# Optimization experiments

Measured on AMD Instinct MI355X. Metric: run time of the kernel, lower is better.

Reference implementation:

```python
import jax, jax.numpy as jnp
import numpy as np

NN_SIZE = 16  # nn_size from __init__


def _knn_idx(points_ref, k):
    """Brute-force KNN of points_ref against itself (replaces faiss_knn).
    Returns (B, N, k) neighbor indices, self point excluded."""
    sq = jnp.sum(points_ref * points_ref, axis=-1)  # (B, N)
    # squared pairwise distances (B, N, N)
    d2 = sq[:, :, None] + sq[:, None, :] - 2.0 * jnp.einsum(
        'bnd,bmd->bnm', points_ref, points_ref)
    _, idx = jax.lax.top_k(-d2, k + 1)  # nearest first; idx[...,0] is self
    return idx[:, :, 1:]


def _edge_lengths(pts, knn_idx):
    """Gather neighbor coords and compute edge lengths (B, N, K)."""
    group = jax.vmap(lambda p, i: p[i])(pts, knn_idx)  # (B, N, K, D)
    return jnp.linalg.norm(group - pts[:, :, None, :], axis=-1)


def setup_inputs() -> dict:
    key = jax.random.key(0)
    k1, k2 = jax.random.split(key)
    B, N, D = 4, 8192, 3
    points_ref = jax.random.normal(k1, (B, N, D), dtype=jnp.float32)
    # pred points: perturbed ref so the loss is non-degenerate
    points = points_ref + 0.01 * jax.random.normal(k2, (B, N, D), dtype=jnp.float32)
    return {"points_ref": points_ref, "points": points}


def reference(points_ref, points):
    # faiss KNN is non-differentiable -> stop_gradient on the index search
    knn_idx = _knn_idx(jax.lax.stop_gradient(points_ref), NN_SIZE)  # (B,N,K)
    dist_ref = _edge_lengths(points_ref, knn_idx)  # (B, N, K)
    dist = _edge_lengths(points, knn_idx)          # (B, N, K)
    # metric = torch.nn.L1Loss() (mean reduction)
    return jnp.mean(jnp.abs(dist_ref - dist))
```

## Files before the change

### kernel.cpp

```cpp
#include <hip/hip_runtime.h>
#include <math.h>

#define BATCH 4
#define NPTS  8192
#define KNN   16
#define KK    17
#define QPB   32
#define SPLITS 8
#define BLOCK 256
#define RANGE (NPTS/SPLITS)
#define SAMPLE 128
#define AL    8
#define CAP   32
#define CHUNK 8
#define TOTAL_EDGES (BATCH*NPTS*KNN)

__global__ void pel_pack(const float* __restrict__ pref, const float* __restrict__ pts,
                         float4* __restrict__ p4r, float4* __restrict__ p4p,
                         float* __restrict__ acc) {
    if (blockIdx.x == 0 && threadIdx.x == 0) acc[0] = 0.0f;
    const int idx = blockIdx.x * blockDim.x + threadIdx.x;
    const int n = BATCH * NPTS;
    if (idx < n) {
        float x = pref[3*idx], y = pref[3*idx+1], z = pref[3*idx+2];
        p4r[idx] = make_float4(x, y, z, fmaf(x, x, fmaf(y, y, z*z)));
        x = pts[3*idx]; y = pts[3*idx+1]; z = pts[3*idx+2];
        p4p[idx] = make_float4(x, y, z, fmaf(x, x, fmaf(y, y, z*z)));
    }
}

__global__ void pel_finalize(const float* __restrict__ acc, float* __restrict__ out) {
    out[0] = acc[0] * (1.0f / (float)TOTAL_EDGES);
}

__device__ __forceinline__ float cand_e4(const float4 p, float xi, float yi, float zi) {
    return fmaf(-2.0f, fmaf(p.x, xi, fmaf(p.y, yi, p.z * zi)), p.w);
}

__global__ __launch_bounds__(BLOCK, 4)
void pel_main(const float4* __restrict__ P4r, const float4* __restrict__ P4p,
              float* __restrict__ acc_ws)
{
    __shared__ float s_c17[KK][BLOCK];
    __shared__ unsigned short s_bufJ[CAP][BLOCK];
    __shared__ float s_tau[QPB];
    __shared__ float s_part[BLOCK / 64];

    const int t  = threadIdx.x;
    const int lq = t & (QPB - 1);
    const int sp = t >> 5;
    const int q  = blockIdx.x * QPB + lq;
    const int b  = q >> 13;
    const int i  = q & (NPTS - 1);

    const float4* __restrict__ Pq = P4r + b * NPTS;
    const float4* __restrict__ Pp = P4p + b * NPTS;

    const float4 self = Pq[i];
    const float xi = self.x, yi = self.y, zi = self.z, sqi = self.w;
    const int base = sp * RANGE;
    const float4* __restrict__ Pb = Pq + base;

    float al[AL];
    #pragma unroll
    for (int k = 0; k < AL; ++k) al[k] = 3.0e38f;
    for (int j0 = 0; j0 < SAMPLE; j0 += CHUNK) {
        float4 c[CHUNK];
        #pragma unroll
        for (int u = 0; u < CHUNK; ++u) c[u] = Pb[j0 + u];
        #pragma unroll
        for (int u = 0; u < CHUNK; ++u) {
            const float e = cand_e4(c[u], xi, yi, zi);
            if (e < al[AL-1]) {
                #pragma unroll
                for (int k = AL-1; k >= 1; --k) al[k] = fminf(al[k], fmaxf(al[k-1], e));
                al[0] = fminf(al[0], e);
            }
        }
    }
    #pragma unroll
    for (int k = 0; k < AL; ++k) s_c17[k][t] = al[k];
    __syncthreads();

    if (t < 64) {
        const int mq = t & 31, half = t >> 5;
        float m[KK];
        #pragma unroll
        for (int k = 0; k < KK; ++k) m[k] = 3.0e38f;
        for (int s = 0; s < SPLITS/2; ++s) {
            const int r = mq + (half * (SPLITS/2) + s) * QPB;
            for (int k = 0; k < AL; ++k) {
                const float c = s_c17[k][r];
                if (c >= m[KK-1]) break;
                #pragma unroll
                for (int kk = KK-1; kk >= 1; --kk) m[kk] = fminf(m[kk], fmaxf(m[kk-1], c));
                m[0] = fminf(m[0], c);
            }
        }
        float tau = -3.0e38f;
        #pragma unroll
        for (int k = 0; k < KK; ++k) {
            const float bk = __shfl(m[KK-1-k], mq + 32, 64);
            tau = fmaxf(tau, fminf(m[k], bk));
        }
        if (half == 0) s_tau[mq] = tau;
    }
    __syncthreads();
    float tauL = s_tau[lq];

    int cnt = 0;
    for (int j0 = 0; j0 < RANGE; j0 += CHUNK) {
        float4 c[CHUNK];
        #pragma unroll
        for (int u = 0; u < CHUNK; ++u) c[u] = Pb[j0 + u];
        #pragma unroll
        for (int u = 0; u < CHUNK; ++u) {
            const float e = cand_e4(c[u], xi, yi, zi);
            if (e <= tauL) {
                s_bufJ[cnt][t] = (unsigned short)(base + j0 + u);
                if (++cnt == CAP) {
                    float c17[KK];
                    #pragma unroll
                    for (int k = 0; k < KK; ++k) c17[k] = 3.0e38f;
                    for (int n = 0; n < CAP; ++n) {
                        const float ee = cand_e4(Pq[s_bufJ[n][t]], xi, yi, zi);
                        if (ee < c17[KK-1]) {
                            #pragma unroll
                            for (int k = KK-1; k >= 1; --k) c17[k] = fminf(c17[k], fmaxf(c17[k-1], ee));
                            c17[0] = fminf(c17[0], ee);
                        }
                    }
                    const float th = c17[KK-1];
                    int kept = 0;
                    for (int n = 0; n < CAP; ++n) {
                        const unsigned short jj = s_bufJ[n][t];
                        const float ee = cand_e4(Pq[jj], xi, yi, zi);
                        if (ee <= th) { s_bufJ[kept][t] = jj; ++kept; }
                    }
                    cnt = kept;
                    tauL = fminf(tauL, th);
                }
            }
        }
    }

    {
        float c17[KK];
        #pragma unroll
        for (int k = 0; k < KK; ++k) c17[k] = 3.0e38f;
        for (int n = 0; n < cnt; ++n) {
            const float ee = cand_e4(Pq[s_bufJ[n][t]], xi, yi, zi);
            if (ee < c17[KK-1]) {
                #pragma unroll
                for (int k = KK-1; k >= 1; --k) c17[k] = fminf(c17[k], fmaxf(c17[k-1], ee));
                c17[0] = fminf(c17[0], ee);
            }
        }
        #pragma unroll
        for (int k = 0; k < KK; ++k) s_c17[k][t] = c17[k];
    }
    __syncthreads();
    if (t < 64) {
        const int mq = t & 31, half = t >> 5;
        float m[KK];
        #pragma unroll
        for (int k = 0; k < KK; ++k) m[k] = 3.0e38f;
        for (int s = 0; s < SPLITS/2; ++s) {
            const int r = mq + (half * (SPLITS/2) + s) * QPB;
            for (int k = 0; k < KK; ++k) {
                const float c = s_c17[k][r];
                if (c >= m[KK-1]) break;
                #pragma unroll
                for (int kk = KK-1; kk >= 1; --kk) m[kk] = fminf(m[kk], fmaxf(m[kk-1], c));
                m[0] = fminf(m[0], c);
            }
        }
        float tau = -3.0e38f;
        #pragma unroll
        for (int k = 0; k < KK; ++k) {
            const float bk = __shfl(m[KK-1-k], mq + 32, 64);
            tau = fmaxf(tau, fminf(m[k], bk));
        }
        if (half == 0) s_tau[mq] = tau;
    }
    __syncthreads();
    const float tau = s_tau[lq];

    const float4 selfp = Pp[i];
    float acc = 0.0f;
    for (int n = 0; n < cnt; ++n) {
        const int jj = s_bufJ[n][t];
        const float ee = cand_e4(Pq[jj], xi, yi, zi);
        if (ee <= tau) {
            const float d2r = fmaxf(ee + sqi, 0.0f);
            const float ep  = cand_e4(Pp[jj], selfp.x, selfp.y, selfp.z);
            const float d2p = fmaxf(ep + selfp.w, 0.0f);
            acc += fabsf(sqrtf(d2r) - sqrtf(d2p));
        }
    }

    #pragma unroll
    for (int off = 32; off > 0; off >>= 1) acc += __shfl_down(acc, off, 64);
    if ((t & 63) == 0) s_part[t >> 6] = acc;
    __syncthreads();
    if (t == 0) {
        float s = 0.0f;
        #pragma unroll
        for (int w = 0; w < BLOCK / 64; ++w) s += s_part[w];
        atomicAdd(acc_ws, s);
    }
}

extern "C" void kernel_launch(void* const* d_in, const int* in_sizes, int n_in,
                              void* d_out, int out_size, void* d_ws, size_t ws_size,
                              hipStream_t stream) {
    const float* pref = (const float*)d_in[0];
    const float* pts  = (const float*)d_in[1];
    float*  wsf = (float*)d_ws;
    float*  acc = wsf;
    float4* P4r = (float4*)(wsf + 4);
    float4* P4p = P4r + BATCH * NPTS;
    float*  out = (float*)d_out;

    const int n = BATCH * NPTS;
    pel_pack<<<(n + 255) / 256, 256, 0, stream>>>(pref, pts, P4r, P4p, acc);
    pel_main<<<n / QPB, BLOCK, 0, stream>>>(P4r, P4p, acc);
    pel_finalize<<<1, 1, 0, stream>>>(acc, out);
}
```

Before: 302.8 us.

## Pack distance and index into sortable keys, branchless candidate buffering, fuse finalize

Candidates become 32-bit keys: the float squared distance with its low 13 mantissa bits replaced by the point index. This lets the top-k lists carry indices directly, so the rescans that reloaded points to recompute distances go away, and the final pass only visits the 17 kept keys. The filter pass writes every key to shared memory and advances the counter without a branch, compacting once the buffer nears capacity. The block shrinks to 16 queries (128 threads), and the finalize kernel is folded into the main kernel through a last-block counter. The truncated mantissa can change neighbor choice on near ties, and unconditional shared stores add write traffic.

```diff
diff --git a/kernel.cpp b/kernel.cpp
--- a/kernel.cpp
+++ b/kernel.cpp
@@ -5,23 +5,26 @@
 #define NPTS  8192
 #define KNN   16
 #define KK    17
-#define QPB   32
+#define QPB   16
 #define SPLITS 8
-#define BLOCK 256
+#define BLOCK (QPB*SPLITS)
 #define RANGE (NPTS/SPLITS)
 #define SAMPLE 128
 #define AL    8
-#define CAP   32
+#define CAP   30
 #define CHUNK 8
+#define NQ    (BATCH*NPTS)
+#define GRID  (NQ/QPB)
+#define JMASK 0x1FFFu
+#define EMASK 0xFFFFE000u
 #define TOTAL_EDGES (BATCH*NPTS*KNN)
 
 __global__ void pel_pack(const float* __restrict__ pref, const float* __restrict__ pts,
                          float4* __restrict__ p4r, float4* __restrict__ p4p,
-                         float* __restrict__ acc) {
-    if (blockIdx.x == 0 && threadIdx.x == 0) acc[0] = 0.0f;
+                         float* __restrict__ acc, unsigned* __restrict__ bcnt) {
+    if (blockIdx.x == 0 && threadIdx.x == 0) { acc[0] = 0.0f; bcnt[0] = 0u; }
     const int idx = blockIdx.x * blockDim.x + threadIdx.x;
-    const int n = BATCH * NPTS;
-    if (idx < n) {
+    if (idx < NQ) {
         float x = pref[3*idx], y = pref[3*idx+1], z = pref[3*idx+2];
         p4r[idx] = make_float4(x, y, z, fmaf(x, x, fmaf(y, y, z*z)));
         x = pts[3*idx]; y = pts[3*idx+1]; z = pts[3*idx+2];
@@ -29,26 +32,50 @@
     }
 }
 
-__global__ void pel_finalize(const float* __restrict__ acc, float* __restrict__ out) {
-    out[0] = acc[0] * (1.0f / (float)TOTAL_EDGES);
-}
-
-__device__ __forceinline__ float cand_e4(const float4 p, float xi, float yi, float zi) {
-    return fmaf(-2.0f, fmaf(p.x, xi, fmaf(p.y, yi, p.z * zi)), p.w);
+__device__ __forceinline__ unsigned mkkey(const float4 p, float xi, float yi,
+                                          float zi, float sqi, unsigned j) {
+    const float dot = fmaf(p.x, xi, fmaf(p.y, yi, p.z * zi));
+    const float d2  = fmaf(-2.0f, dot, p.w) + sqi;
+    return (__float_as_uint(d2) & EMASK) | j;
+}
+
+template<int RL>
+__device__ __forceinline__ unsigned merge_tau(const unsigned (*s_key)[BLOCK], int t) {
+    const int mq = t & (QPB - 1), half = t >> 4;
+    unsigned m[KK];
+    #pragma unroll
+    for (int k = 0; k < KK; ++k) m[k] = 0xFFFFFFFFu;
+    for (int s = (SPLITS/2) * half; s < (SPLITS/2) * (half + 1); ++s) {
+        const int col = mq + s * QPB;
+        for (int k = 0; k < RL; ++k) {
+            const unsigned c = s_key[k][col];
+            if (c >= m[KK-1]) break;
+            #pragma unroll
+            for (int kk = KK-1; kk >= 1; --kk) m[kk] = min(m[kk], max(m[kk-1], c));
+            m[0] = min(m[0], c);
+        }
+    }
+    unsigned tau = 0;
+    #pragma unroll
+    for (int k = 0; k < KK; ++k) {
+        const unsigned bk = (unsigned)__shfl((int)m[KK-1-k], t ^ 16, 64);
+        tau = max(tau, min(m[k], bk));
+    }
+    return tau;
 }
 
 __global__ __launch_bounds__(BLOCK, 4)
 void pel_main(const float4* __restrict__ P4r, const float4* __restrict__ P4p,
-              float* __restrict__ acc_ws)
+              float* __restrict__ acc_ws, unsigned* __restrict__ bcnt,
+              float* __restrict__ out)
 {
-    __shared__ float s_c17[KK][BLOCK];
-    __shared__ unsigned short s_bufJ[CAP][BLOCK];
-    __shared__ float s_tau[QPB];
+    __shared__ unsigned s_key[CAP][BLOCK];
+    __shared__ unsigned s_tau[QPB];
     __shared__ float s_part[BLOCK / 64];
 
     const int t  = threadIdx.x;
     const int lq = t & (QPB - 1);
-    const int sp = t >> 5;
+    const int sp = t >> 4;
     const int q  = blockIdx.x * QPB + lq;
     const int b  = q >> 13;
     const int i  = q & (NPTS - 1);
@@ -58,55 +85,33 @@
 
     const float4 self = Pq[i];
     const float xi = self.x, yi = self.y, zi = self.z, sqi = self.w;
-    const int base = sp * RANGE;
+    const unsigned base = (unsigned)(sp * RANGE);
     const float4* __restrict__ Pb = Pq + base;
 
-    float al[AL];
-    #pragma unroll
-    for (int k = 0; k < AL; ++k) al[k] = 3.0e38f;
+    unsigned al[AL];
+    #pragma unroll
+    for (int k = 0; k < AL; ++k) al[k] = 0xFFFFFFFFu;
     for (int j0 = 0; j0 < SAMPLE; j0 += CHUNK) {
         float4 c[CHUNK];
         #pragma unroll
         for (int u = 0; u < CHUNK; ++u) c[u] = Pb[j0 + u];
         #pragma unroll
         for (int u = 0; u < CHUNK; ++u) {
-            const float e = cand_e4(c[u], xi, yi, zi);
-            if (e < al[AL-1]) {
-                #pragma unroll
-                for (int k = AL-1; k >= 1; --k) al[k] = fminf(al[k], fmaxf(al[k-1], e));
-                al[0] = fminf(al[0], e);
-            }
-        }
-    }
-    #pragma unroll
-    for (int k = 0; k < AL; ++k) s_c17[k][t] = al[k];
-    __syncthreads();
-
-    if (t < 64) {
-        const int mq = t & 31, half = t >> 5;
-        float m[KK];
-        #pragma unroll
-        for (int k = 0; k < KK; ++k) m[k] = 3.0e38f;
-        for (int s = 0; s < SPLITS/2; ++s) {
-            const int r = mq + (half * (SPLITS/2) + s) * QPB;
-            for (int k = 0; k < AL; ++k) {
-                const float c = s_c17[k][r];
-                if (c >= m[KK-1]) break;
-                #pragma unroll
-                for (int kk = KK-1; kk >= 1; --kk) m[kk] = fminf(m[kk], fmaxf(m[kk-1], c));
-                m[0] = fminf(m[0], c);
-            }
-        }
-        float tau = -3.0e38f;
-        #pragma unroll
-        for (int k = 0; k < KK; ++k) {
-            const float bk = __shfl(m[KK-1-k], mq + 32, 64);
-            tau = fmaxf(tau, fminf(m[k], bk));
-        }
-        if (half == 0) s_tau[mq] = tau;
-    }
-    __syncthreads();
-    float tauL = s_tau[lq];
+            const unsigned key = mkkey(c[u], xi, yi, zi, sqi, base + j0 + u);
+            #pragma unroll
+            for (int k = AL-1; k >= 1; --k) al[k] = min(al[k], max(al[k-1], key));
+            al[0] = min(al[0], key);
+        }
+    }
+    #pragma unroll
+    for (int k = 0; k < AL; ++k) s_key[k][t] = al[k];
+    __syncthreads();
+    if (t < 2 * QPB) {
+        const unsigned tau0 = merge_tau<AL>(s_key, t);
+        if ((t >> 4) == 0) s_tau[t & (QPB-1)] = tau0;
+    }
+    __syncthreads();
+    unsigned tauL = s_tau[lq];
 
     int cnt = 0;
     for (int j0 = 0; j0 < RANGE; j0 += CHUNK) {
@@ -115,99 +120,81 @@
         for (int u = 0; u < CHUNK; ++u) c[u] = Pb[j0 + u];
         #pragma unroll
         for (int u = 0; u < CHUNK; ++u) {
-            const float e = cand_e4(c[u], xi, yi, zi);
-            if (e <= tauL) {
-                s_bufJ[cnt][t] = (unsigned short)(base + j0 + u);
-                if (++cnt == CAP) {
-                    float c17[KK];
-                    #pragma unroll
-                    for (int k = 0; k < KK; ++k) c17[k] = 3.0e38f;
-                    for (int n = 0; n < CAP; ++n) {
-                        const float ee = cand_e4(Pq[s_bufJ[n][t]], xi, yi, zi);
-                        if (ee < c17[KK-1]) {
-                            #pragma unroll
-                            for (int k = KK-1; k >= 1; --k) c17[k] = fminf(c17[k], fmaxf(c17[k-1], ee));
-                            c17[0] = fminf(c17[0], ee);
-                        }
-                    }
-                    const float th = c17[KK-1];
-                    int kept = 0;
-                    for (int n = 0; n < CAP; ++n) {
-                        const unsigned short jj = s_bufJ[n][t];
-                        const float ee = cand_e4(Pq[jj], xi, yi, zi);
-                        if (ee <= th) { s_bufJ[kept][t] = jj; ++kept; }
-                    }
-                    cnt = kept;
-                    tauL = fminf(tauL, th);
-                }
+            const unsigned key = mkkey(c[u], xi, yi, zi, sqi, base + j0 + u);
+            s_key[cnt][t] = key;
+            cnt += (key <= tauL) ? 1 : 0;
+        }
+        if (cnt > CAP - CHUNK) {
+            unsigned k17[KK];
+            #pragma unroll
+            for (int k = 0; k < KK; ++k) k17[k] = 0xFFFFFFFFu;
+            for (int n = 0; n < cnt; ++n) {
+                const unsigned c2 = s_key[n][t];
+                #pragma unroll
+                for (int k = KK-1; k >= 1; --k) k17[k] = min(k17[k], max(k17[k-1], c2));
+                k17[0] = min(k17[0], c2);
             }
-        }
-    }
-
-    {
-        float c17[KK];
-        #pragma unroll
-        for (int k = 0; k < KK; ++k) c17[k] = 3.0e38f;
-        for (int n = 0; n < cnt; ++n) {
-            const float ee = cand_e4(Pq[s_bufJ[n][t]], xi, yi, zi);
-            if (ee < c17[KK-1]) {
-                #pragma unroll
-                for (int k = KK-1; k >= 1; --k) c17[k] = fminf(c17[k], fmaxf(c17[k-1], ee));
-                c17[0] = fminf(c17[0], ee);
+            const unsigned th = k17[KK-1];
+            int kept = 0;
+            for (int n = 0; n < cnt; ++n) {
+                const unsigned c2 = s_key[n][t];
+                if (c2 <= th) { s_key[kept][t] = c2; ++kept; }
             }
-        }
-        #pragma unroll
-        for (int k = 0; k < KK; ++k) s_c17[k][t] = c17[k];
-    }
-    __syncthreads();
-    if (t < 64) {
-        const int mq = t & 31, half = t >> 5;
-        float m[KK];
-        #pragma unroll
-        for (int k = 0; k < KK; ++k) m[k] = 3.0e38f;
-        for (int s = 0; s < SPLITS/2; ++s) {
-            const int r = mq + (half * (SPLITS/2) + s) * QPB;
-            for (int k = 0; k < KK; ++k) {
-                const float c = s_c17[k][r];
-                if (c >= m[KK-1]) break;
-                #pragma unroll
-                for (int kk = KK-1; kk >= 1; --kk) m[kk] = fminf(m[kk], fmaxf(m[kk-1], c));
-                m[0] = fminf(m[0], c);
-            }
-        }
-        float tau = -3.0e38f;
-        #pragma unroll
-        for (int k = 0; k < KK; ++k) {
-            const float bk = __shfl(m[KK-1-k], mq + 32, 64);
-            tau = fmaxf(tau, fminf(m[k], bk));
-        }
-        if (half == 0) s_tau[mq] = tau;
-    }
-    __syncthreads();
-    const float tau = s_tau[lq];
+            cnt = kept;
+            tauL = min(tauL, th);
+        }
+    }
+
+    unsigned c17[KK];
+    #pragma unroll
+    for (int k = 0; k < KK; ++k) c17[k] = 0xFFFFFFFFu;
+    for (int n = 0; n < cnt; ++n) {
+        const unsigned c2 = s_key[n][t];
+        #pragma unroll
+        for (int k = KK-1; k >= 1; --k) c17[k] = min(c17[k], max(c17[k-1], c2));
+        c17[0] = min(c17[0], c2);
+    }
+    __syncthreads();
+    #pragma unroll
+    for (int k = 0; k < KK; ++k) s_key[k][t] = c17[k];
+    __syncthreads();
+    if (t < 2 * QPB) {
+        const unsigned tauX = merge_tau<KK>(s_key, t);
+        if ((t >> 4) == 0) s_tau[t & (QPB-1)] = tauX;
+    }
+    __syncthreads();
+    const unsigned tauK = s_tau[lq];
 
     const float4 selfp = Pp[i];
-    float acc = 0.0f;
-    for (int n = 0; n < cnt; ++n) {
-        const int jj = s_bufJ[n][t];
-        const float ee = cand_e4(Pq[jj], xi, yi, zi);
-        if (ee <= tau) {
-            const float d2r = fmaxf(ee + sqi, 0.0f);
-            const float ep  = cand_e4(Pp[jj], selfp.x, selfp.y, selfp.z);
-            const float d2p = fmaxf(ep + selfp.w, 0.0f);
-            acc += fabsf(sqrtf(d2r) - sqrtf(d2p));
-        }
-    }
-
-    #pragma unroll
-    for (int off = 32; off > 0; off >>= 1) acc += __shfl_down(acc, off, 64);
-    if ((t & 63) == 0) s_part[t >> 6] = acc;
+    float accv = 0.0f;
+    #pragma unroll
+    for (int k = 0; k < KK; ++k) {
+        if (c17[k] <= tauK) {
+            const int j = (int)(c17[k] & JMASK);
+            const float4 pr = Pq[j];
+            const float dotr = fmaf(pr.x, xi, fmaf(pr.y, yi, pr.z * zi));
+            const float d2r  = fmaxf(fmaf(-2.0f, dotr, pr.w) + sqi, 0.0f);
+            const float4 pp = Pp[j];
+            const float dotp = fmaf(pp.x, selfp.x, fmaf(pp.y, selfp.y, pp.z * selfp.z));
+            const float d2p  = fmaxf(fmaf(-2.0f, dotp, pp.w) + selfp.w, 0.0f);
+            accv += fabsf(sqrtf(d2r) - sqrtf(d2p));
+        }
+    }
+
+    #pragma unroll
+    for (int off = 32; off > 0; off >>= 1) accv += __shfl_down(accv, off, 64);
+    if ((t & 63) == 0) s_part[t >> 6] = accv;
     __syncthreads();
     if (t == 0) {
-        float s = 0.0f;
-        #pragma unroll
-        for (int w = 0; w < BLOCK / 64; ++w) s += s_part[w];
+        const float s = s_part[0] + s_part[1];
         atomicAdd(acc_ws, s);
+        __threadfence();
+        const unsigned old = atomicAdd(bcnt, 1u);
+        if (old == GRID - 1) {
+            __threadfence();
+            const float total = atomicAdd(acc_ws, 0.0f);
+            out[0] = total * (1.0f / (float)TOTAL_EDGES);
+        }
     }
 }
 
@@ -216,14 +203,12 @@
                               hipStream_t stream) {
     const float* pref = (const float*)d_in[0];
     const float* pts  = (const float*)d_in[1];
-    float*  wsf = (float*)d_ws;
-    float*  acc = wsf;
-    float4* P4r = (float4*)(wsf + 4);
-    float4* P4p = P4r + BATCH * NPTS;
-    float*  out = (float*)d_out;
-
-    const int n = BATCH * NPTS;
-    pel_pack<<<(n + 255) / 256, 256, 0, stream>>>(pref, pts, P4r, P4p, acc);
-    pel_main<<<n / QPB, BLOCK, 0, stream>>>(P4r, P4p, acc);
-    pel_finalize<<<1, 1, 0, stream>>>(acc, out);
-}
+    float*    acc  = (float*)d_ws;
+    unsigned* bcnt = (unsigned*)d_ws + 1;
+    float4*   P4r  = (float4*)((char*)d_ws + 16);
+    float4*   P4p  = P4r + NQ;
+    float*    out  = (float*)d_out;
+
+    pel_pack<<<(NQ + 255) / 256, 256, 0, stream>>>(pref, pts, P4r, P4p, acc, bcnt);
+    pel_main<<<GRID, BLOCK, 0, stream>>>(P4r, P4p, acc, bcnt, out);
+}
```

Result: slower. 320.9 us (+6.0%).
